# Performance work log

Measured on AMD Instinct MI355X. Metric: run time of the kernel, lower is better.

Reference implementation:

```python
import jax, jax.numpy as jnp
import numpy as np

DECAY = 0.8
EPS = 1e-7
K = 1024  # codebook_size
D = 128   # dim


def setup_inputs() -> dict:
    key = jax.random.key(0)
    k1, k2, k3 = jax.random.split(key, 3)
    x = jax.random.normal(k1, (8, 32768, D), dtype=jnp.float32)
    embed = jax.random.normal(k2, (K, D), dtype=jnp.float32)
    ema_embed = jax.random.normal(k3, (K, D), dtype=jnp.float32)
    ema_num = jnp.ones((K,), dtype=jnp.float32)
    return {"x": x, "embed": embed, "ema_embed": ema_embed, "ema_num": ema_num}


def reference(x, embed, ema_embed, ema_num):
    # Flatten all leading dims: [..., d] -> [N, d]
    flatten = x.reshape(-1, D)
    # Negative squared euclidean distance: -(||f||^2 - 2 f E^T + ||e||^2)
    f2 = jnp.sum(flatten * flatten, axis=1, keepdims=True)          # [N, 1]
    e2 = jnp.sum(embed * embed, axis=1)                              # [K]
    distance = -(f2 - 2.0 * (flatten @ embed.T) + e2)                # [N, K]
    embed_ind = jnp.argmax(distance, axis=-1)                        # [N]
    quantize = embed[embed_ind].reshape(x.shape)                     # [..., d]

    # EMA update (training path); onehot.sum(0) == bincount, flatten^T @ onehot == segment_sum
    counts = jax.ops.segment_sum(jnp.ones_like(embed_ind, dtype=jnp.float32), embed_ind, num_segments=K)  # [K]
    sums = jax.ops.segment_sum(flatten, embed_ind, num_segments=K)   # [K, D]
    ema_num_new = DECAY * ema_num + (1.0 - DECAY) * counts
    ema_embed_new = DECAY * ema_embed + (1.0 - DECAY) * sums

    # laplace smoothing * total (ema_num_threshold <= 0 path)
    total = jnp.sum(ema_num_new)
    smoothed = (ema_num_new + EPS) / (total + K * EPS) * total
    embed_new = ema_embed_new / smoothed[:, None]                    # [K, D]

    return quantize, embed_new, ema_num_new, ema_embed_new
```

## Files before the change

### kernel.cpp

```cpp
#include <hip/hip_runtime.h>

#define N_TOTAL (8 * 32768)
#define D 128
#define K 1024
#define DECAY 0.8f
#define EPS 1e-7f
#define MARGIN 4e-3f

typedef __attribute__((ext_vector_type(8))) short bf16x8;
typedef __attribute__((ext_vector_type(4))) float f32x4;
union B8 { uint4 u; bf16x8 b; };

#define MFMA(A, B, C) __builtin_amdgcn_mfma_f32_16x16x32_bf16((A), (B), (C), 0, 0, 0)

#define PASS(EHL, X, A0, A1, A2, A3)                        \
    {                                                       \
        B8 a_, b_;                                          \
        a_.u = EHL[0]; b_.u = X[0]; A0 = MFMA(a_.b, b_.b, A0); \
        a_.u = EHL[1]; b_.u = X[1]; A1 = MFMA(a_.b, b_.b, A1); \
        a_.u = EHL[2]; b_.u = X[2]; A2 = MFMA(a_.b, b_.b, A2); \
        a_.u = EHL[3]; b_.u = X[3]; A3 = MFMA(a_.b, b_.b, A3); \
    }

__device__ inline unsigned short f2b(float v, float& back) {
    unsigned int u = __float_as_uint(v);
    unsigned int r = (u + 0x7FFFu + ((u >> 16) & 1u)) >> 16;
    back = __uint_as_float(r << 16);
    return (unsigned short)r;
}

__global__ __launch_bounds__(128) void k_prep(
    const float* __restrict__ embed, unsigned short* __restrict__ ehi,
    unsigned short* __restrict__ elo, float* __restrict__ e2h) {
    __shared__ float r2[2];
    int c = blockIdx.x, tid = threadIdx.x;
    float v = embed[(size_t)c * D + tid];
    float hb;
    unsigned short h = f2b(v, hb);
    float lb;
    unsigned short l = f2b(v - hb, lb);
    ehi[(size_t)c * D + tid] = h;
    elo[(size_t)c * D + tid] = l;
    float sq = v * v;
    for (int off = 32; off; off >>= 1) sq += __shfl_down(sq, off, 64);
    if ((tid & 63) == 0) r2[tid >> 6] = sq;
    __syncthreads();
    if (tid == 0) e2h[c] = 0.5f * (r2[0] + r2[1]);
}

__global__ __launch_bounds__(256) void k_zero(unsigned int* __restrict__ counts,
                                              unsigned int* __restrict__ rescue_cnt,
                                              float* __restrict__ gsum) {
    int i = blockIdx.x * 256 + threadIdx.x;
    if (i < K) counts[i] = 0u;
    if (i == 0) *rescue_cnt = 0u;
    gsum[i] = 0.f;
}

__global__ __launch_bounds__(512, 2) void k_screen(
    const float* __restrict__ x, const uint4* __restrict__ ehi4,
    const uint4* __restrict__ elo4, const float* __restrict__ e2h,
    unsigned int* __restrict__ ind, unsigned int* __restrict__ rescue_cnt,
    unsigned int* __restrict__ rescue_list) {
    __shared__ uint4 ebh[2][64 * 17];
    __shared__ uint4 ebl[2][64 * 17];
    __shared__ float e2s[K];

    int tid = threadIdx.x;
    int w = tid >> 6, lane = tid & 63;
    int l15 = lane & 15, q = lane >> 4;
    size_t row = (size_t)blockIdx.x * 128 + w * 16 + l15;

    for (int i = tid; i < K; i += 512) e2s[i] = e2h[i];

    uint4 xh[4], xl[4];
    const float* xp = x + row * D + q * 8;
#pragma unroll
    for (int j = 0; j < 4; j++) {
        float4 f0 = *(const float4*)(xp + j * 32);
        float4 f1 = *(const float4*)(xp + j * 32 + 4);
        float fs[8] = {f0.x, f0.y, f0.z, f0.w, f1.x, f1.y, f1.z, f1.w};
        unsigned int hh[4], ll[4];
#pragma unroll
        for (int p = 0; p < 4; p++) {
            float b0, b1, d0, d1;
            unsigned short h0 = f2b(fs[2 * p], b0);
            unsigned short h1 = f2b(fs[2 * p + 1], b1);
            unsigned short s0 = f2b(fs[2 * p] - b0, d0);
            unsigned short s1 = f2b(fs[2 * p + 1] - b1, d1);
            hh[p] = (unsigned int)h0 | ((unsigned int)h1 << 16);
            ll[p] = (unsigned int)s0 | ((unsigned int)s1 << 16);
        }
        xh[j] = make_uint4(hh[0], hh[1], hh[2], hh[3]);
        xl[j] = make_uint4(ll[0], ll[1], ll[2], ll[3]);
    }

    {
        int i0 = tid, i1 = tid + 512;
        int c0 = i0 >> 4, u0 = i0 & 15;
        int c1 = i1 >> 4, u1 = i1 & 15;
        ebh[0][c0 * 17 + u0] = ehi4[i0];
        ebl[0][c0 * 17 + u0] = elo4[i0];
        ebh[0][c1 * 17 + u1] = ehi4[i1];
        ebl[0][c1 * 17 + u1] = elo4[i1];
    }
    __syncthreads();

    float t1 = -1e30f, t2 = -1e30f;
    unsigned int i1g = 0u;

    for (int st = 0; st < 16; st++) {
        int b = st & 1;
        uint4 rh0, rl0, rh1, rl1;
        if (st < 15) {
            const uint4* gh = ehi4 + (size_t)(st + 1) * 1024;
            const uint4* gl = elo4 + (size_t)(st + 1) * 1024;
            rh0 = gh[tid];
            rl0 = gl[tid];
            rh1 = gh[tid + 512];
            rl1 = gl[tid + 512];
        }

#pragma unroll
        for (int ct = 0; ct < 4; ct++) {
            uint4 eh[4], el[4];
            int cr = (ct * 16 + l15) * 17;
#pragma unroll
            for (int j = 0; j < 4; j++) {
                eh[j] = ebh[b][cr + 4 * j + q];
                el[j] = ebl[b][cr + 4 * j + q];
            }
            f32x4 a0 = {0.f, 0.f, 0.f, 0.f}, a1 = {0.f, 0.f, 0.f, 0.f};
            f32x4 a2 = {0.f, 0.f, 0.f, 0.f}, a3 = {0.f, 0.f, 0.f, 0.f};
            PASS(eh, xh, a0, a1, a2, a3);
            PASS(el, xh, a0, a1, a2, a3);
            PASS(eh, xl, a0, a1, a2, a3);
            f32x4 sv = (a0 + a1) + (a2 + a3);
            int cbase = st * 64 + ct * 16 + q * 4;
            float4 e2q = *(const float4*)&e2s[cbase];
            float vv[4] = {sv.x - e2q.x, sv.y - e2q.y, sv.z - e2q.z,
                           sv.w - e2q.w};
#pragma unroll
            for (int r = 0; r < 4; r++) {
                float u = vv[r];
                unsigned int c = (unsigned int)(cbase + r);
                bool gt = u > t1;
                t2 = fmaxf(t2, fminf(t1, u));
                t1 = fmaxf(t1, u);
                i1g = gt ? c : i1g;
            }
        }

        if (st < 15) {
            int i0 = tid, i1 = tid + 512;
            int c0 = i0 >> 4, u0 = i0 & 15;
            int c1 = i1 >> 4, u1 = i1 & 15;
            ebh[b ^ 1][c0 * 17 + u0] = rh0;
            ebl[b ^ 1][c0 * 17 + u0] = rl0;
            ebh[b ^ 1][c1 * 17 + u1] = rh1;
            ebl[b ^ 1][c1 * 17 + u1] = rl1;
        }
        __syncthreads();
    }

#pragma unroll
    for (int off = 16; off <= 32; off <<= 1) {
        float t1p = __shfl_xor(t1, off);
        float t2p = __shfl_xor(t2, off);
        unsigned int i1p = (unsigned int)__shfl_xor((int)i1g, off);
        float nt2 = fmaxf(fminf(t1, t1p), fmaxf(t2, t2p));
        unsigned int ni1 = (t1p > t1 || (t1p == t1 && i1p < i1g)) ? i1p : i1g;
        t1 = fmaxf(t1, t1p);
        t2 = nt2;
        i1g = ni1;
    }
    if (lane < 16) {
        ind[row] = i1g;
        if (t1 - t2 < MARGIN) {
            unsigned int pos = atomicAdd(rescue_cnt, 1u);
            rescue_list[pos] = (unsigned int)row;
        }
    }
}

__global__ __launch_bounds__(256) void k_rescue(
    const unsigned int* __restrict__ rescue_cnt,
    const unsigned int* __restrict__ rescue_list, const float* __restrict__ x,
    const float* __restrict__ embed, const float* __restrict__ e2h,
    unsigned int* __restrict__ ind) {
    __shared__ float xr[D];
    __shared__ float bv[4];
    __shared__ unsigned int bi[4];
    unsigned int cnt = *rescue_cnt;
    int tid = threadIdx.x;
    for (unsigned int it = blockIdx.x; it < cnt; it += gridDim.x) {
        unsigned int row = rescue_list[it];
        __syncthreads();
        if (tid < D) xr[tid] = x[(size_t)row * D + tid];
        __syncthreads();
        float best = -1e30f;
        unsigned int besti = 0u;
        for (int c = tid; c < K; c += 256) {
            const float* e = embed + (size_t)c * D;
            float s = 0.f;
            for (int d = 0; d < D; d += 4) {
                float4 xv = *(const float4*)&xr[d];
                float4 ev = *(const float4*)&e[d];
                s += xv.x * ev.x + xv.y * ev.y + xv.z * ev.z + xv.w * ev.w;
            }
            s -= e2h[c];
            if (s > best) { best = s; besti = (unsigned int)c; }
        }
        for (int off = 32; off; off >>= 1) {
            float ov = __shfl_down(best, off, 64);
            unsigned int oi = (unsigned int)__shfl_down((int)besti, off, 64);
            if (ov > best || (ov == best && oi < besti)) { best = ov; besti = oi; }
        }
        if ((tid & 63) == 0) { bv[tid >> 6] = best; bi[tid >> 6] = besti; }
        __syncthreads();
        if (tid == 0) {
            for (int wv = 1; wv < 4; wv++)
                if (bv[wv] > best || (bv[wv] == best && bi[wv] < besti)) {
                    best = bv[wv];
                    besti = bi[wv];
                }
            ind[row] = besti;
        }
    }
}

__global__ __launch_bounds__(256) void k_quant(
    const unsigned int* __restrict__ ind, const float* __restrict__ embed,
    float* __restrict__ q) {
    size_t gid = (size_t)blockIdx.x * 256 + threadIdx.x;
    size_t n = gid >> 5;
    int d4 = (int)(gid & 31) << 2;
    unsigned int c = ind[n];
    *(float4*)&q[n * D + d4] = *(const float4*)&embed[(size_t)c * D + d4];
}

__global__ __launch_bounds__(256) void k_count(
    const unsigned int* __restrict__ ind, unsigned int* __restrict__ counts) {
    __shared__ unsigned int hist[K];
    int tid = threadIdx.x;
    for (int i = tid; i < K; i += 256) hist[i] = 0u;
    __syncthreads();
    int base = blockIdx.x * 1024;
#pragma unroll
    for (int j = 0; j < 4; j++)
        atomicAdd(&hist[ind[base + j * 256 + tid]], 1u);
    __syncthreads();
    for (int i = tid; i < K; i += 256) {
        unsigned int h = hist[i];
        if (h) atomicAdd(&counts[i], h);
    }
}

__global__ __launch_bounds__(1024) void k_scan(
    const unsigned int* __restrict__ counts, unsigned int* __restrict__ cursor) {
    __shared__ unsigned int tmp[K];
    int tid = threadIdx.x;
    unsigned int v = counts[tid];
    tmp[tid] = v;
    __syncthreads();
    for (int off = 1; off < K; off <<= 1) {
        unsigned int t = (tid >= off) ? tmp[tid - off] : 0u;
        __syncthreads();
        tmp[tid] += t;
        __syncthreads();
    }
    cursor[tid] = tmp[tid] - v;
}

__global__ __launch_bounds__(256) void k_scatter(
    const unsigned int* __restrict__ ind, unsigned int* __restrict__ cursor,
    unsigned int* __restrict__ bucket) {
    unsigned int n = blockIdx.x * 256 + threadIdx.x;
    unsigned int c = ind[n];
    unsigned int pos = atomicAdd(&cursor[c], 1u);
    bucket[pos] = (n << 10) | c;
}

__global__ __launch_bounds__(128) void k_sum2(
    const unsigned int* __restrict__ bucket, const float* __restrict__ x,
    float* __restrict__ gsum) {
    __shared__ unsigned int ent[128];
    int tid = threadIdx.x;
    ent[tid] = bucket[blockIdx.x * 128 + tid];
    __syncthreads();
    float acc = 0.f;
    unsigned int cur = ent[0] & 1023u;
    for (int e = 0; e < 128; e++) {
        unsigned int pk = ent[e];
        unsigned int c = pk & 1023u;
        unsigned int n = pk >> 10;
        if (c != cur) {
            atomicAdd(&gsum[(size_t)cur * D + tid], acc);
            acc = 0.f;
            cur = c;
        }
        acc += x[(size_t)n * D + tid];
    }
    atomicAdd(&gsum[(size_t)cur * D + tid], acc);
}

__global__ __launch_bounds__(256) void k_emafin(
    const float* __restrict__ gsum, const unsigned int* __restrict__ counts,
    const float* __restrict__ ema_num, const float* __restrict__ ema_embed,
    float* __restrict__ ema_num_new, float* __restrict__ ema_embed_new) {
    int gid = blockIdx.x * 256 + threadIdx.x;
    ema_embed_new[gid] = DECAY * ema_embed[gid] + (1.0f - DECAY) * gsum[gid];
    if (gid < K)
        ema_num_new[gid] =
            DECAY * ema_num[gid] + (1.0f - DECAY) * (float)counts[gid];
}

__global__ __launch_bounds__(1024) void k_denom(
    const float* __restrict__ ema_num_new, float* __restrict__ denom) {
    __shared__ float red[16];
    int tid = threadIdx.x;
    float v = ema_num_new[tid];
    float s = v;
    for (int off = 32; off; off >>= 1) s += __shfl_down(s, off, 64);
    if ((tid & 63) == 0) red[tid >> 6] = s;
    __syncthreads();
    if (tid < 16) {
        float t = red[tid];
        for (int off = 8; off; off >>= 1) t += __shfl_down(t, off, 16);
        if (tid == 0) red[0] = t;
    }
    __syncthreads();
    float total = red[0];
    denom[tid] = (v + EPS) / (total + (float)K * EPS) * total;
}

__global__ __launch_bounds__(256) void k_embednew(
    const float* __restrict__ ema_embed_new, const float* __restrict__ denom,
    float* __restrict__ embed_new) {
    int gid = blockIdx.x * 256 + threadIdx.x;
    int k = gid >> 5;
    int d4 = (gid & 31) << 2;
    float4 v = *(const float4*)&ema_embed_new[(size_t)k * D + d4];
    float s = denom[k];
    float4 o;
    o.x = v.x / s; o.y = v.y / s; o.z = v.z / s; o.w = v.w / s;
    *(float4*)&embed_new[(size_t)k * D + d4] = o;
}

extern "C" void kernel_launch(void* const* d_in, const int* in_sizes, int n_in,
                              void* d_out, int out_size, void* d_ws,
                              size_t ws_size, hipStream_t stream) {
    const float* x = (const float*)d_in[0];
    const float* embed = (const float*)d_in[1];
    const float* ema_embed = (const float*)d_in[2];
    const float* ema_num = (const float*)d_in[3];

    float* out = (float*)d_out;
    float* quantize = out;
    float* embed_new = out + (size_t)N_TOTAL * D;
    float* ema_num_new = embed_new + (size_t)K * D;
    float* ema_embed_new = ema_num_new + K;

    char* ws = (char*)d_ws;
    unsigned int* ind = (unsigned int*)ws;
    unsigned int* bucket = ind + N_TOTAL;
    unsigned int* rescue_list = bucket + N_TOTAL;
    unsigned short* ehi = (unsigned short*)(rescue_list + N_TOTAL);
    unsigned short* elo = ehi + (size_t)K * D;
    float* gsum = (float*)(elo + (size_t)K * D);
    float* e2h = gsum + (size_t)K * D;
    float* denom = e2h + K;
    unsigned int* counts = (unsigned int*)(denom + K);
    unsigned int* cursor = counts + K;
    unsigned int* rescue_cnt = cursor + K;

    k_prep<<<K, 128, 0, stream>>>(embed, ehi, elo, e2h);
    k_zero<<<(K * D) / 256, 256, 0, stream>>>(counts, rescue_cnt, gsum);
    k_screen<<<N_TOTAL / 128, 512, 0, stream>>>(
        x, (const uint4*)ehi, (const uint4*)elo, e2h, ind, rescue_cnt,
        rescue_list);
    k_rescue<<<256, 256, 0, stream>>>(rescue_cnt, rescue_list, x, embed, e2h,
                                      ind);
    k_quant<<<(N_TOTAL * 32) / 256, 256, 0, stream>>>(ind, embed, quantize);
    k_count<<<N_TOTAL / 1024, 256, 0, stream>>>(ind, counts);
    k_scan<<<1, K, 0, stream>>>(counts, cursor);
    k_scatter<<<N_TOTAL / 256, 256, 0, stream>>>(ind, cursor, bucket);
    k_sum2<<<N_TOTAL / 128, 128, 0, stream>>>(bucket, x, gsum);
    k_emafin<<<(K * D) / 256, 256, 0, stream>>>(gsum, counts, ema_num,
                                                ema_embed, ema_num_new,
                                                ema_embed_new);
    k_denom<<<1, K, 0, stream>>>(ema_num_new, denom);
    k_embednew<<<(K * D / 4) / 256, 256, 0, stream>>>(ema_embed_new, denom,
                                                      embed_new);
}
```

Before: 633.5 us.

## Process two row tiles per wave in screen kernel to reuse codebook fragments

Each wave in the screening kernel now handles two 16-row tiles instead of one, and the block shrinks from 512 to 256 threads while still covering 128 rows. Every codebook fragment read from LDS feeds twice as many MFMAs, which halves LDS read traffic per MFMA. Each thread also stages four global codebook chunks per stage instead of two. The cost is roughly double the register use for x fragments and accumulators, which may cut occupancy, and fewer waves per block to hide latency.

```diff
diff --git a/kernel.cpp b/kernel.cpp
--- a/kernel.cpp
+++ b/kernel.cpp
@@ -27,6 +27,29 @@
     unsigned int r = (u + 0x7FFFu + ((u >> 16) & 1u)) >> 16;
     back = __uint_as_float(r << 16);
     return (unsigned short)r;
+}
+
+__device__ __forceinline__ void load_x(const float* __restrict__ xp,
+                                       uint4* XH, uint4* XL) {
+#pragma unroll
+    for (int j = 0; j < 4; j++) {
+        float4 f0 = *(const float4*)(xp + j * 32);
+        float4 f1 = *(const float4*)(xp + j * 32 + 4);
+        float fs[8] = {f0.x, f0.y, f0.z, f0.w, f1.x, f1.y, f1.z, f1.w};
+        unsigned int hh[4], ll[4];
+#pragma unroll
+        for (int p = 0; p < 4; p++) {
+            float b0, b1, d0, d1;
+            unsigned short h0 = f2b(fs[2 * p], b0);
+            unsigned short h1 = f2b(fs[2 * p + 1], b1);
+            unsigned short s0 = f2b(fs[2 * p] - b0, d0);
+            unsigned short s1 = f2b(fs[2 * p + 1] - b1, d1);
+            hh[p] = (unsigned int)h0 | ((unsigned int)h1 << 16);
+            ll[p] = (unsigned int)s0 | ((unsigned int)s1 << 16);
+        }
+        XH[j] = make_uint4(hh[0], hh[1], hh[2], hh[3]);
+        XL[j] = make_uint4(ll[0], ll[1], ll[2], ll[3]);
+    }
 }
 
 __global__ __launch_bounds__(128) void k_prep(
@@ -57,7 +80,7 @@
     gsum[i] = 0.f;
 }
 
-__global__ __launch_bounds__(512, 2) void k_screen(
+__global__ __launch_bounds__(256, 2) void k_screen(
     const float* __restrict__ x, const uint4* __restrict__ ehi4,
     const uint4* __restrict__ elo4, const float* __restrict__ e2h,
     unsigned int* __restrict__ ind, unsigned int* __restrict__ rescue_cnt,
@@ -69,56 +92,38 @@
     int tid = threadIdx.x;
     int w = tid >> 6, lane = tid & 63;
     int l15 = lane & 15, q = lane >> 4;
-    size_t row = (size_t)blockIdx.x * 128 + w * 16 + l15;
-
-    for (int i = tid; i < K; i += 512) e2s[i] = e2h[i];
-
-    uint4 xh[4], xl[4];
-    const float* xp = x + row * D + q * 8;
-#pragma unroll
-    for (int j = 0; j < 4; j++) {
-        float4 f0 = *(const float4*)(xp + j * 32);
-        float4 f1 = *(const float4*)(xp + j * 32 + 4);
-        float fs[8] = {f0.x, f0.y, f0.z, f0.w, f1.x, f1.y, f1.z, f1.w};
-        unsigned int hh[4], ll[4];
-#pragma unroll
-        for (int p = 0; p < 4; p++) {
-            float b0, b1, d0, d1;
-            unsigned short h0 = f2b(fs[2 * p], b0);
-            unsigned short h1 = f2b(fs[2 * p + 1], b1);
-            unsigned short s0 = f2b(fs[2 * p] - b0, d0);
-            unsigned short s1 = f2b(fs[2 * p + 1] - b1, d1);
-            hh[p] = (unsigned int)h0 | ((unsigned int)h1 << 16);
-            ll[p] = (unsigned int)s0 | ((unsigned int)s1 << 16);
-        }
-        xh[j] = make_uint4(hh[0], hh[1], hh[2], hh[3]);
-        xl[j] = make_uint4(ll[0], ll[1], ll[2], ll[3]);
-    }
-
-    {
-        int i0 = tid, i1 = tid + 512;
-        int c0 = i0 >> 4, u0 = i0 & 15;
-        int c1 = i1 >> 4, u1 = i1 & 15;
-        ebh[0][c0 * 17 + u0] = ehi4[i0];
-        ebl[0][c0 * 17 + u0] = elo4[i0];
-        ebh[0][c1 * 17 + u1] = ehi4[i1];
-        ebl[0][c1 * 17 + u1] = elo4[i1];
-    }
-    __syncthreads();
-
-    float t1 = -1e30f, t2 = -1e30f;
-    unsigned int i1g = 0u;
+    size_t rowA = (size_t)blockIdx.x * 128 + w * 32 + l15;
+    size_t rowB = rowA + 16;
+
+    for (int i = tid; i < K; i += 256) e2s[i] = e2h[i];
+
+    uint4 xh0[4], xl0[4], xh1[4], xl1[4];
+    load_x(x + rowA * D + q * 8, xh0, xl0);
+    load_x(x + rowB * D + q * 8, xh1, xl1);
+
+#pragma unroll
+    for (int k2 = 0; k2 < 4; k2++) {
+        int i = tid + k2 * 256;
+        int c = i >> 4, u = i & 15;
+        ebh[0][c * 17 + u] = ehi4[i];
+        ebl[0][c * 17 + u] = elo4[i];
+    }
+    __syncthreads();
+
+    float t1a = -1e30f, t2a = -1e30f, t1b = -1e30f, t2b = -1e30f;
+    unsigned int i1a = 0u, i1b = 0u;
 
     for (int st = 0; st < 16; st++) {
         int b = st & 1;
-        uint4 rh0, rl0, rh1, rl1;
+        uint4 rh[4], rl[4];
         if (st < 15) {
             const uint4* gh = ehi4 + (size_t)(st + 1) * 1024;
             const uint4* gl = elo4 + (size_t)(st + 1) * 1024;
-            rh0 = gh[tid];
-            rl0 = gl[tid];
-            rh1 = gh[tid + 512];
-            rl1 = gl[tid + 512];
+#pragma unroll
+            for (int k2 = 0; k2 < 4; k2++) {
+                rh[k2] = gh[tid + k2 * 256];
+                rl[k2] = gl[tid + k2 * 256];
+            }
         }
 
 #pragma unroll
@@ -132,53 +137,83 @@
             }
             f32x4 a0 = {0.f, 0.f, 0.f, 0.f}, a1 = {0.f, 0.f, 0.f, 0.f};
             f32x4 a2 = {0.f, 0.f, 0.f, 0.f}, a3 = {0.f, 0.f, 0.f, 0.f};
-            PASS(eh, xh, a0, a1, a2, a3);
-            PASS(el, xh, a0, a1, a2, a3);
-            PASS(eh, xl, a0, a1, a2, a3);
-            f32x4 sv = (a0 + a1) + (a2 + a3);
+            PASS(eh, xh0, a0, a1, a2, a3);
+            PASS(el, xh0, a0, a1, a2, a3);
+            PASS(eh, xl0, a0, a1, a2, a3);
+            f32x4 c0 = {0.f, 0.f, 0.f, 0.f}, c1 = {0.f, 0.f, 0.f, 0.f};
+            f32x4 c2 = {0.f, 0.f, 0.f, 0.f}, c3 = {0.f, 0.f, 0.f, 0.f};
+            PASS(eh, xh1, c0, c1, c2, c3);
+            PASS(el, xh1, c0, c1, c2, c3);
+            PASS(eh, xl1, c0, c1, c2, c3);
+
             int cbase = st * 64 + ct * 16 + q * 4;
             float4 e2q = *(const float4*)&e2s[cbase];
-            float vv[4] = {sv.x - e2q.x, sv.y - e2q.y, sv.z - e2q.z,
-                           sv.w - e2q.w};
+            f32x4 svA = (a0 + a1) + (a2 + a3);
+            f32x4 svB = (c0 + c1) + (c2 + c3);
+            float vvA[4] = {svA.x - e2q.x, svA.y - e2q.y, svA.z - e2q.z,
+                            svA.w - e2q.w};
+            float vvB[4] = {svB.x - e2q.x, svB.y - e2q.y, svB.z - e2q.z,
+                            svB.w - e2q.w};
 #pragma unroll
             for (int r = 0; r < 4; r++) {
-                float u = vv[r];
                 unsigned int c = (unsigned int)(cbase + r);
-                bool gt = u > t1;
-                t2 = fmaxf(t2, fminf(t1, u));
-                t1 = fmaxf(t1, u);
-                i1g = gt ? c : i1g;
+                float uA = vvA[r];
+                bool gA = uA > t1a;
+                t2a = fmaxf(t2a, fminf(t1a, uA));
+                t1a = fmaxf(t1a, uA);
+                i1a = gA ? c : i1a;
+                float uB = vvB[r];
+                bool gB = uB > t1b;
+                t2b = fmaxf(t2b, fminf(t1b, uB));
+                t1b = fmaxf(t1b, uB);
+                i1b = gB ? c : i1b;
             }
         }
 
         if (st < 15) {
-            int i0 = tid, i1 = tid + 512;
-            int c0 = i0 >> 4, u0 = i0 & 15;
-            int c1 = i1 >> 4, u1 = i1 & 15;
-            ebh[b ^ 1][c0 * 17 + u0] = rh0;
-            ebl[b ^ 1][c0 * 17 + u0] = rl0;
-            ebh[b ^ 1][c1 * 17 + u1] = rh1;
-            ebl[b ^ 1][c1 * 17 + u1] = rl1;
+#pragma unroll
+            for (int k2 = 0; k2 < 4; k2++) {
+                int i = tid + k2 * 256;
+                int c = i >> 4, u = i & 15;
+                ebh[b ^ 1][c * 17 + u] = rh[k2];
+                ebl[b ^ 1][c * 17 + u] = rl[k2];
+            }
         }
         __syncthreads();
     }
 
 #pragma unroll
     for (int off = 16; off <= 32; off <<= 1) {
-        float t1p = __shfl_xor(t1, off);
-        float t2p = __shfl_xor(t2, off);
-        unsigned int i1p = (unsigned int)__shfl_xor((int)i1g, off);
-        float nt2 = fmaxf(fminf(t1, t1p), fmaxf(t2, t2p));
-        unsigned int ni1 = (t1p > t1 || (t1p == t1 && i1p < i1g)) ? i1p : i1g;
-        t1 = fmaxf(t1, t1p);
-        t2 = nt2;
-        i1g = ni1;
+        float t1p = __shfl_xor(t1a, off);
+        float t2p = __shfl_xor(t2a, off);
+        unsigned int i1p = (unsigned int)__shfl_xor((int)i1a, off);
+        float nt2 = fmaxf(fminf(t1a, t1p), fmaxf(t2a, t2p));
+        unsigned int ni1 = (t1p > t1a || (t1p == t1a && i1p < i1a)) ? i1p : i1a;
+        t1a = fmaxf(t1a, t1p);
+        t2a = nt2;
+        i1a = ni1;
+    }
+#pragma unroll
+    for (int off = 16; off <= 32; off <<= 1) {
+        float t1p = __shfl_xor(t1b, off);
+        float t2p = __shfl_xor(t2b, off);
+        unsigned int i1p = (unsigned int)__shfl_xor((int)i1b, off);
+        float nt2 = fmaxf(fminf(t1b, t1p), fmaxf(t2b, t2p));
+        unsigned int ni1 = (t1p > t1b || (t1p == t1b && i1p < i1b)) ? i1p : i1b;
+        t1b = fmaxf(t1b, t1p);
+        t2b = nt2;
+        i1b = ni1;
     }
     if (lane < 16) {
-        ind[row] = i1g;
-        if (t1 - t2 < MARGIN) {
+        ind[rowA] = i1a;
+        if (t1a - t2a < MARGIN) {
             unsigned int pos = atomicAdd(rescue_cnt, 1u);
-            rescue_list[pos] = (unsigned int)row;
+            rescue_list[pos] = (unsigned int)rowA;
+        }
+        ind[rowB] = i1b;
+        if (t1b - t2b < MARGIN) {
+            unsigned int pos = atomicAdd(rescue_cnt, 1u);
+            rescue_list[pos] = (unsigned int)rowB;
         }
     }
 }
@@ -376,7 +411,7 @@
 
     k_prep<<<K, 128, 0, stream>>>(embed, ehi, elo, e2h);
     k_zero<<<(K * D) / 256, 256, 0, stream>>>(counts, rescue_cnt, gsum);
-    k_screen<<<N_TOTAL / 128, 512, 0, stream>>>(
+    k_screen<<<N_TOTAL / 128, 256, 0, stream>>>(
         x, (const uint4*)ehi, (const uint4*)elo, e2h, ind, rescue_cnt,
         rescue_list);
     k_rescue<<<256, 256, 0, stream>>>(rescue_cnt, rescue_list, x, embed, e2h,
```

After: 761.4 us. 1.2x slower.
